# Kernel optimization log

Measured on AMD Instinct MI355X. Metric: run time of the kernel, lower is better.

Reference implementation:

```python
import jax, jax.numpy as jnp
import numpy as np

NUM_HEADS = 4
NUM_POINTS = 8


def deform_attn_3d(q, value, ref, Hf, Wf, Wv, bv, Wo, bo, Wa, ba):
    # q: (BS,N,C)  value: (BS,Hf*Wf,C)  ref: (BS,N,D,2) normalized (x,y) in [0,1]
    BS, N, C = q.shape
    H, P = NUM_HEADS, NUM_POINTS
    D = ref.shape[2]
    c = C // H
    # value projection, split heads: (BS,H,M,c)
    v = (value @ Wv + bv).reshape(BS, Hf * Wf, H, c).transpose(0, 2, 1, 3)
    # sampling offsets and attention weights from the query
    off = (q @ Wo + bo).reshape(BS, N, H, P, 2)
    attn = jax.nn.softmax((q @ Wa + ba).reshape(BS, N, H, P), axis=-1)
    # normalize offsets by (W,H); distribute P points over D z-anchors (P//D per anchor)
    norm = jnp.array([Wf, Hf], dtype=q.dtype)
    off = off.reshape(BS, N, H, P // D, D, 2) / norm
    loc = (ref[:, :, None, None, :, :] + off).reshape(BS, N, H, P, 2)
    # grid_sample(align_corners=False, padding=zeros): pixel = loc*size - 0.5
    x = loc[..., 0] * Wf - 0.5
    y = loc[..., 1] * Hf - 0.5
    x0f = jnp.floor(x)
    y0f = jnp.floor(y)
    lx = x - x0f
    ly = y - y0f
    x0 = x0f.astype(jnp.int32)
    y0 = y0f.astype(jnp.int32)

    def tohead(a):  # (BS,N,H,P) -> (BS,H,N*P)
        return a.transpose(0, 2, 1, 3).reshape(BS, H, N * P)

    def gather(yy, xx):
        valid = ((xx >= 0) & (xx < Wf) & (yy >= 0) & (yy < Hf)).astype(q.dtype)
        idx = jnp.clip(yy, 0, Hf - 1) * Wf + jnp.clip(xx, 0, Wf - 1)
        g = jnp.take_along_axis(v, tohead(idx)[..., None], axis=2)  # (BS,H,N*P,c)
        return g * tohead(valid)[..., None]

    out = (gather(y0, x0) * tohead((1 - lx) * (1 - ly))[..., None]
           + gather(y0, x0 + 1) * tohead(lx * (1 - ly))[..., None]
           + gather(y0 + 1, x0) * tohead((1 - lx) * ly)[..., None]
           + gather(y0 + 1, x0 + 1) * tohead(lx * ly)[..., None])
    out = (out * tohead(attn)[..., None]).reshape(BS, H, N, P, c).sum(3)  # (BS,H,N,c)
    return out.transpose(0, 2, 1, 3).reshape(BS, N, C)


def spatial_cross_attention(query, query_pos, value, reference_points_cam, bev_mask,
                            Hf, Wf, Wv, bv, Wo, bo, Wa, ba, Wout, bout):
    # query/query_pos: (B,N,C); value: (S,M,B,C); ref: (S,B,N,D,2); bev_mask: (S,B,N,D)
    B, N, C = query.shape
    S, M = value.shape[0], value.shape[1]
    D = reference_points_cam.shape[3]
    q = query + query_pos
    # broadcast queries over cameras (mask-equivalent of the torch rebatch/compaction):
    # deformable attention is per-query independent, so computing all queries per cam
    # and masking invalid ones is the same math as rebatch+scatter.
    q_all = jnp.broadcast_to(q[:, None], (B, S, N, C)).reshape(B * S, N, C)
    v_all = value.transpose(2, 0, 1, 3).reshape(B * S, M, C)
    ref = reference_points_cam.transpose(1, 0, 2, 3, 4).reshape(B * S, N, D, 2)
    out = deform_attn_3d(q_all, v_all, ref, Hf, Wf, Wv, bv, Wo, bo, Wa, ba)
    out = out.reshape(B, S, N, C)
    mask_q = (bev_mask.sum(-1) > 0).astype(query.dtype)  # (S,B,N): query hits this cam
    slots = (out * mask_q.transpose(1, 0, 2)[..., None]).sum(1)  # (B,N,C)
    count = jnp.maximum(mask_q.sum(0), 1.0)  # (B,N) clamp(min=1)
    slots = slots / count[..., None]
    # output_proj, dropout (eval -> identity), residual with original query
    return slots @ Wout + bout + query


def setup_inputs() -> dict:
    B, S, N, Z, C = 1, 6, 16384, 8, 128
    Hf, Wf = 28, 50
    H, P = NUM_HEADS, NUM_POINTS
    rng = jax.random.key(0)
    ks = jax.random.split(rng, 12)
    return {
        "query": jax.random.normal(ks[0], (B, N, C), jnp.float32),
        "query_pos": 0.1 * jax.random.normal(ks[1], (B, N, C), jnp.float32),
        "value": jax.random.normal(ks[2], (S, Hf * Wf, B, C), jnp.float32),
        "reference_points_cam": jax.random.uniform(ks[3], (S, B, N, Z, 2), jnp.float32),
        "bev_mask": jax.random.randint(ks[4], (S, B, N, Z), 0, 2).astype(bool),
        "Wv": 0.02 * jax.random.normal(ks[5], (C, C), jnp.float32),
        "bv": jnp.zeros((C,), jnp.float32),
        "Wo": 0.02 * jax.random.normal(ks[6], (C, H * P * 2), jnp.float32),
        "bo": 0.5 * jax.random.normal(ks[7], (H * P * 2,), jnp.float32),
        "Wa": 0.02 * jax.random.normal(ks[8], (C, H * P), jnp.float32),
        "ba": jnp.zeros((H * P,), jnp.float32),
        "Wout": 0.02 * jax.random.normal(ks[9], (C, C), jnp.float32),
        "bout": jnp.zeros((C,), jnp.float32),
        "Hf": Hf,
        "Wf": Wf,
    }


def reference(query, query_pos, value, reference_points_cam, bev_mask,
              Wv, bv, Wo, bo, Wa, ba, Wout, bout, Hf, Wf):
    return spatial_cross_attention(query, query_pos, value, reference_points_cam, bev_mask,
                                   Hf, Wf, Wv, bv, Wo, bo, Wa, ba, Wout, bout)
```

## Files before the change

kernel.cpp:

```cpp
#include <hip/hip_runtime.h>

#define N_Q   16384
#define C_DIM 128
#define S_CAM 6
#define M_VAL 1400
#define D_Z   8
#define HF    28
#define WF    50
#define QPB   16

typedef float f32x2 __attribute__((ext_vector_type(2)));

__device__ __forceinline__ bool mask_any(const unsigned char* __restrict__ mask,
                                         int mflag, size_t mbase){
  if(mflag==0){
    int any=0;
    #pragma unroll
    for(int d=0;d<D_Z;d++) any |= mask[mbase+d];
    return any!=0;
  } else if(mflag==1){
    const int* mp = (const int*)mask;  int any=0;
    #pragma unroll
    for(int d=0;d<D_Z;d++) any |= mp[mbase+d];
    return any!=0;
  } else {
    const long long* mp = (const long long*)mask;  long long any=0;
    #pragma unroll
    for(int d=0;d<D_Z;d++) any |= mp[mbase+d];
    return any!=0;
  }
}

__device__ __forceinline__ void corner_acc(const uint4 cv, const float wgt,
                                           float* __restrict__ acc){
  const unsigned dw[4] = {cv.x, cv.y, cv.z, cv.w};
  #pragma unroll
  for(int j=0;j<4;j++){
    const f32x2 lo = __builtin_amdgcn_cvt_pk_f32_fp8(dw[j], false);
    const f32x2 hi = __builtin_amdgcn_cvt_pk_f32_fp8(dw[j], true);
    acc[j*4+0] += wgt*lo[0];  acc[j*4+1] += wgt*lo[1];
    acc[j*4+2] += wgt*hi[0];  acc[j*4+3] += wgt*hi[1];
  }
}

__global__ __launch_bounds__(256)
void value_proj_kernel(const float* __restrict__ value,
                       const float* __restrict__ Wv,
                       const float* __restrict__ bv,
                       unsigned char* __restrict__ v8,
                       const unsigned char* __restrict__ mask,
                       int* __restrict__ flag){
  __shared__ float tile[8][C_DIM];
  __shared__ int s_cntA, s_cntB;
  const int tid = threadIdx.x;
  const int col = tid & 127;
  const int rh  = tid >> 7;
  const int r0  = blockIdx.x * 8;
  if(blockIdx.x==0 && tid==0){ s_cntA=0; s_cntB=0; }
  {
    const float4* src = (const float4*)(value + (size_t)r0*C_DIM);
    ((float4*)&tile[0][0])[tid] = src[tid];
  }
  __syncthreads();
  float acc[4];
  const float bias = bv[col];
  #pragma unroll
  for(int r=0;r<4;r++) acc[r]=bias;
  for(int k=0;k<C_DIM;k+=4){
    const float w0 = Wv[(k+0)*C_DIM + col];
    const float w1 = Wv[(k+1)*C_DIM + col];
    const float w2 = Wv[(k+2)*C_DIM + col];
    const float w3 = Wv[(k+3)*C_DIM + col];
    #pragma unroll
    for(int r=0;r<4;r++){
      const float4 t = *(const float4*)&tile[rh*4+r][k];
      acc[r] += t.x*w0 + t.y*w1 + t.z*w2 + t.w*w3;
    }
  }
  #pragma unroll
  for(int r=0;r<4;r++){
    const int pk = __builtin_amdgcn_cvt_pk_fp8_f32(acc[r], acc[r], 0, false);
    v8[(size_t)(r0+rh*4+r)*C_DIM + col] = (unsigned char)(pk & 0xff);
  }
  if(blockIdx.x==0){
    int a=0, b=0;
    for(int i=tid;i<1024;i+=256){
      const unsigned char v = mask[i];
      if(((i&3)!=0) && v) a=1;
      if(((i&7)==4) && v) b=1;
    }
    if(a) atomicOr(&s_cntA,1);
    if(b) atomicOr(&s_cntB,1);
    __syncthreads();
    if(tid==0) flag[0] = s_cntA ? 0 : (s_cntB ? 1 : 2);
  }
}

__global__ __launch_bounds__(256)
void fused_deform_kernel(const unsigned char* __restrict__ v8,
                         const float* __restrict__ query,
                         const float* __restrict__ query_pos,
                         const float* __restrict__ Wo, const float* __restrict__ bo,
                         const float* __restrict__ Wa, const float* __restrict__ ba,
                         const float* __restrict__ ref,
                         const unsigned char* __restrict__ mask,
                         const int* __restrict__ flag,
                         const float* __restrict__ Wout,
                         const float* __restrict__ bout,
                         float* __restrict__ out){
  __shared__ float  qs[QPB][C_DIM+4];
  __shared__ float  offs[QPB][68];
  __shared__ float  attns[QPB][36];
  __shared__ float  logits[QPB][36];
  __shared__ float2 refs[QPB][S_CAM*D_Z+1];
  __shared__ int    activ[QPB][S_CAM];
  __shared__ float  cinv[QPB];

  const int tid = threadIdx.x;
  const int n0  = blockIdx.x * QPB;
  const int mflag = flag[0];
  const int qi = tid >> 4;
  const int l  = tid & 15;

  float2 rpre[3];
  #pragma unroll
  for(int j=0;j<3;j++){
    const int e = tid + 256*j;
    const int q = e/48, r = e%48;
    rpre[j] = ((const float2*)ref)[((size_t)(r>>3)*N_Q + (n0+q))*D_Z + (r&7)];
  }

  {
    const float4* qa = (const float4*)(query     + (size_t)n0*C_DIM);
    const float4* qb = (const float4*)(query_pos + (size_t)n0*C_DIM);
    #pragma unroll
    for(int j=0;j<2;j++){
      const int idx = tid + 256*j;
      const int r = idx >> 5, c4 = idx & 31;
      float4 A = qa[idx], B = qb[idx];
      *(float4*)&qs[r][c4*4] = make_float4(A.x+B.x, A.y+B.y, A.z+B.z, A.w+B.w);
    }
  }
  __syncthreads();

  {
    float ao0 = bo[l*4+0], ao1 = bo[l*4+1], ao2 = bo[l*4+2], ao3 = bo[l*4+3];
    float aa0 = ba[l*2+0], aa1 = ba[l*2+1];
    for(int k=0;k<C_DIM;k++){
      const float qv = qs[qi][k];
      const float4 wo = *(const float4*)&Wo[k*64 + l*4];
      const float2 wa = *(const float2*)&Wa[k*32 + l*2];
      ao0 += qv*wo.x; ao1 += qv*wo.y; ao2 += qv*wo.z; ao3 += qv*wo.w;
      aa0 += qv*wa.x; aa1 += qv*wa.y;
    }
    offs[qi][l*4+0] = ao0;  offs[qi][l*4+1] = ao1;
    offs[qi][l*4+2] = ao2;  offs[qi][l*4+3] = ao3;
    logits[qi][l*2+0] = aa0;  logits[qi][l*2+1] = aa1;
  }
  #pragma unroll
  for(int j=0;j<3;j++){
    const int e = tid + 256*j;
    refs[e/48][e%48] = rpre[j];
  }
  if(tid < QPB*S_CAM){
    const int q2 = tid / S_CAM, s = tid % S_CAM;
    activ[q2][s] = mask_any(mask, mflag, ((size_t)s*N_Q + (n0+q2))*D_Z) ? 1 : 0;
  }
  __syncthreads();
  if(tid < 64){
    const int q2 = tid >> 2, h = tid & 3;
    const float* L = &logits[q2][h*8];
    float mx = L[0];
    #pragma unroll
    for(int p=1;p<8;p++) mx = fmaxf(mx, L[p]);
    float e[8], ssum = 0.f;
    #pragma unroll
    for(int p=0;p<8;p++){ e[p] = __expf(L[p]-mx); ssum += e[p]; }
    const float inv = 1.f/ssum;
    #pragma unroll
    for(int p=0;p<8;p++) attns[q2][h*8+p] = e[p]*inv;
  } else if(tid >= 256-QPB){
    const int q2 = tid - (256-QPB);
    int c = 0;
    #pragma unroll
    for(int s=0;s<S_CAM;s++) c += activ[q2][s];
    cinv[q2] = 1.f / fmaxf((float)c, 1.f);
  }
  __syncthreads();

  const int sg  = l >> 3;
  const int ll  = l & 7;
  const int gch = ll*16;
  const int gh  = ll >> 1;
  float acc[16];
  #pragma unroll
  for(int i=0;i<16;i++) acc[i]=0.f;

  for(int s=sg*3; s<sg*3+3; s++){
    if(!activ[qi][s]) continue;
    const unsigned char* vb = v8 + (size_t)s*M_VAL*C_DIM + gch;
    #pragma unroll 2
    for(int p=0;p<8;p++){
      const float2 r2 = refs[qi][s*8+p];
      const float ox = offs[qi][gh*16+p*2+0];
      const float oy = offs[qi][gh*16+p*2+1];
      const float x = fmaf(r2.x, (float)WF, ox - 0.5f);
      const float y = fmaf(r2.y, (float)HF, oy - 0.5f);
      const float x0f = floorf(x), y0f = floorf(y);
      const float fx = x - x0f,    fy = y - y0f;
      const int x0 = (int)x0f, y0 = (int)y0f;
      const int x1 = x0+1,     y1 = y0+1;
      const float at = attns[qi][gh*8+p];
      const float wx0 = (x0>=0 && x0<WF) ? (1.f-fx) : 0.f;
      const float wx1 = (x1>=0 && x1<WF) ? fx       : 0.f;
      const float wy0 = ((y0>=0 && y0<HF) ? (1.f-fy) : 0.f) * at;
      const float wy1 = ((y1>=0 && y1<HF) ? fy       : 0.f) * at;
      const int x0c = min(max(x0,0), WF-1), x1c = min(max(x1,0), WF-1);
      const int y0c = min(max(y0,0), HF-1), y1c = min(max(y1,0), HF-1);
      const float w00 = wx0*wy0, w01 = wx1*wy0, w10 = wx0*wy1, w11 = wx1*wy1;
      const uint4 c00 = *(const uint4*)(vb + (size_t)(y0c*WF+x0c)*C_DIM);
      const uint4 c01 = *(const uint4*)(vb + (size_t)(y0c*WF+x1c)*C_DIM);
      const uint4 c10 = *(const uint4*)(vb + (size_t)(y1c*WF+x0c)*C_DIM);
      const uint4 c11 = *(const uint4*)(vb + (size_t)(y1c*WF+x1c)*C_DIM);
      corner_acc(c00, w00, acc);
      corner_acc(c01, w01, acc);
      corner_acc(c10, w10, acc);
      corner_acc(c11, w11, acc);
    }
  }

  __syncthreads();
  if(sg==0){
    #pragma unroll
    for(int i=0;i<4;i++)
      *(float4*)&qs[qi][gch+i*4] = *(const float4*)&acc[i*4];
  }
  __syncthreads();
  if(sg==1){
    const float inv = cinv[qi];
    #pragma unroll
    for(int i=0;i<4;i++){
      float4 pA = *(const float4*)&qs[qi][gch+i*4];
      *(float4*)&qs[qi][gch+i*4] = make_float4((pA.x+acc[i*4+0])*inv,
                                               (pA.y+acc[i*4+1])*inv,
                                               (pA.z+acc[i*4+2])*inv,
                                               (pA.w+acc[i*4+3])*inv);
    }
  }
  __syncthreads();
  {
    const int c0 = l*8;
    const int n  = n0 + qi;
    const float4 bA = *(const float4*)&bout[c0];
    const float4 bB = *(const float4*)&bout[c0+4];
    const float4 rA = *(const float4*)&query[(size_t)n*C_DIM + c0];
    const float4 rB = *(const float4*)&query[(size_t)n*C_DIM + c0 + 4];
    float o0=bA.x+rA.x, o1=bA.y+rA.y, o2=bA.z+rA.z, o3=bA.w+rA.w;
    float o4=bB.x+rB.x, o5=bB.y+rB.y, o6=bB.z+rB.z, o7=bB.w+rB.w;
    for(int k=0;k<C_DIM;k++){
      const float sv = qs[qi][k];
      const float4 wA = *(const float4*)&Wout[(size_t)k*C_DIM + c0];
      const float4 wB = *(const float4*)&Wout[(size_t)k*C_DIM + c0 + 4];
      o0 += sv*wA.x; o1 += sv*wA.y; o2 += sv*wA.z; o3 += sv*wA.w;
      o4 += sv*wB.x; o5 += sv*wB.y; o6 += sv*wB.z; o7 += sv*wB.w;
    }
    *(float4*)&out[(size_t)n*C_DIM + c0]     = make_float4(o0,o1,o2,o3);
    *(float4*)&out[(size_t)n*C_DIM + c0 + 4] = make_float4(o4,o5,o6,o7);
  }
}

extern "C" void kernel_launch(void* const* d_in, const int* in_sizes, int n_in,
                              void* d_out, int out_size, void* d_ws, size_t ws_size,
                              hipStream_t stream){
  const float* query     = (const float*)d_in[0];
  const float* query_pos = (const float*)d_in[1];
  const float* value     = (const float*)d_in[2];
  const float* ref       = (const float*)d_in[3];
  const unsigned char* mask = (const unsigned char*)d_in[4];
  const float* Wv   = (const float*)d_in[5];
  const float* bv   = (const float*)d_in[6];
  const float* Wo   = (const float*)d_in[7];
  const float* bo   = (const float*)d_in[8];
  const float* Wa   = (const float*)d_in[9];
  const float* ba   = (const float*)d_in[10];
  const float* Wout = (const float*)d_in[11];
  const float* bout = (const float*)d_in[12];
  float* out = (float*)d_out;

  int* flag = (int*)d_ws;
  unsigned char* v8 = (unsigned char*)((char*)d_ws + 64);

  value_proj_kernel<<<(S_CAM*M_VAL)/8, 256, 0, stream>>>(value, Wv, bv, v8, mask, flag);
  fused_deform_kernel<<<N_Q/QPB, 256, 0, stream>>>(v8, query, query_pos,
                                                   Wo, bo, Wa, ba, ref, mask, flag,
                                                   Wout, bout, out);
}
```

Measured before the change: 186.5 us.

## Stage per-head camera feature maps in LDS and split output projection into separate kernel

Restructures the gather so each block handles 128 queries for a single head and stages each camera's fp8 value slice for that head in shared memory, turning random global corner loads into LDS reads. The sampled, count-normalized result is written as fp16 to a workspace buffer, and a new out_proj kernel applies Wout, the bias and the residual. The goal is to cut scattered global/L2 gather traffic, at the cost of one extra kernel launch, an fp16 round trip through memory, repeated per-camera LDS fills, and larger LDS use per block that lowers occupancy. Camera masking now zeroes the attention weights instead of skipping the camera, so every camera's work is executed.

```diff
diff --git a/kernel.cpp b/kernel.cpp
--- a/kernel.cpp
+++ b/kernel.cpp
@@ -1,4 +1,5 @@
 #include <hip/hip_runtime.h>
+#include <hip/hip_fp16.h>
 
 #define N_Q   16384
 #define C_DIM 128
@@ -7,7 +8,8 @@
 #define D_Z   8
 #define HF    28
 #define WF    50
-#define QPB   16
+#define QT    128
+#define CSTR  48
 
 typedef float f32x2 __attribute__((ext_vector_type(2)));
 
@@ -97,79 +99,66 @@
 }
 
 __global__ __launch_bounds__(256)
-void fused_deform_kernel(const unsigned char* __restrict__ v8,
-                         const float* __restrict__ query,
-                         const float* __restrict__ query_pos,
-                         const float* __restrict__ Wo, const float* __restrict__ bo,
-                         const float* __restrict__ Wa, const float* __restrict__ ba,
-                         const float* __restrict__ ref,
-                         const unsigned char* __restrict__ mask,
-                         const int* __restrict__ flag,
-                         const float* __restrict__ Wout,
-                         const float* __restrict__ bout,
-                         float* __restrict__ out){
-  __shared__ float  qs[QPB][C_DIM+4];
-  __shared__ float  offs[QPB][68];
-  __shared__ float  attns[QPB][36];
-  __shared__ float  logits[QPB][36];
-  __shared__ float2 refs[QPB][S_CAM*D_Z+1];
-  __shared__ int    activ[QPB][S_CAM];
-  __shared__ float  cinv[QPB];
+void gather_kernel(const unsigned char* __restrict__ v8,
+                   const float* __restrict__ query,
+                   const float* __restrict__ query_pos,
+                   const float* __restrict__ Wo, const float* __restrict__ bo,
+                   const float* __restrict__ Wa, const float* __restrict__ ba,
+                   const float* __restrict__ ref,
+                   const unsigned char* __restrict__ mask,
+                   const int* __restrict__ flag,
+                   unsigned short* __restrict__ slots16){
+  __shared__ union {
+    struct {
+      float qsL[32][132];
+      float logitsL[128][9];
+    } pre;
+    unsigned char cam[M_VAL*CSTR];
+  } U;
+  __shared__ float offsL[128][17];
+  __shared__ float attnL[128][8];
+  __shared__ float cinvL[128];
+  __shared__ unsigned char activL[128][8];
 
   const int tid = threadIdx.x;
-  const int n0  = blockIdx.x * QPB;
+  const int h   = blockIdx.x & 3;
+  const int n0  = (blockIdx.x >> 2) * QT;
   const int mflag = flag[0];
-  const int qi = tid >> 4;
-  const int l  = tid & 15;
-
-  float2 rpre[3];
-  #pragma unroll
-  for(int j=0;j<3;j++){
-    const int e = tid + 256*j;
-    const int q = e/48, r = e%48;
-    rpre[j] = ((const float2*)ref)[((size_t)(r>>3)*N_Q + (n0+q))*D_Z + (r&7)];
-  }
-
-  {
-    const float4* qa = (const float4*)(query     + (size_t)n0*C_DIM);
-    const float4* qb = (const float4*)(query_pos + (size_t)n0*C_DIM);
-    #pragma unroll
-    for(int j=0;j<2;j++){
-      const int idx = tid + 256*j;
-      const int r = idx >> 5, c4 = idx & 31;
-      float4 A = qa[idx], B = qb[idx];
-      *(float4*)&qs[r][c4*4] = make_float4(A.x+B.x, A.y+B.y, A.z+B.z, A.w+B.w);
-    }
-  }
-  __syncthreads();
-
-  {
-    float ao0 = bo[l*4+0], ao1 = bo[l*4+1], ao2 = bo[l*4+2], ao3 = bo[l*4+3];
-    float aa0 = ba[l*2+0], aa1 = ba[l*2+1];
-    for(int k=0;k<C_DIM;k++){
-      const float qv = qs[qi][k];
-      const float4 wo = *(const float4*)&Wo[k*64 + l*4];
-      const float2 wa = *(const float2*)&Wa[k*32 + l*2];
-      ao0 += qv*wo.x; ao1 += qv*wo.y; ao2 += qv*wo.z; ao3 += qv*wo.w;
-      aa0 += qv*wa.x; aa1 += qv*wa.y;
-    }
-    offs[qi][l*4+0] = ao0;  offs[qi][l*4+1] = ao1;
-    offs[qi][l*4+2] = ao2;  offs[qi][l*4+3] = ao3;
-    logits[qi][l*2+0] = aa0;  logits[qi][l*2+1] = aa1;
-  }
-  #pragma unroll
-  for(int j=0;j<3;j++){
-    const int e = tid + 256*j;
-    refs[e/48][e%48] = rpre[j];
-  }
-  if(tid < QPB*S_CAM){
-    const int q2 = tid / S_CAM, s = tid % S_CAM;
-    activ[q2][s] = mask_any(mask, mflag, ((size_t)s*N_Q + (n0+q2))*D_Z) ? 1 : 0;
-  }
-  __syncthreads();
-  if(tid < 64){
-    const int q2 = tid >> 2, h = tid & 3;
-    const float* L = &logits[q2][h*8];
+
+  const int pq = tid >> 3;
+  const int pj = tid & 7;
+  for(int c=0;c<4;c++){
+    {
+      const float4* qa = (const float4*)(query     + (size_t)(n0 + c*32)*C_DIM);
+      const float4* qb = (const float4*)(query_pos + (size_t)(n0 + c*32)*C_DIM);
+      #pragma unroll
+      for(int i=0;i<4;i++){
+        const int idx = tid + 256*i;
+        const int r = idx >> 5, cc = idx & 31;
+        float4 A = qa[idx], B = qb[idx];
+        *(float4*)&U.pre.qsL[r][cc*4] = make_float4(A.x+B.x, A.y+B.y, A.z+B.z, A.w+B.w);
+      }
+    }
+    __syncthreads();
+    {
+      float ao0 = bo[h*16 + pj*2], ao1 = bo[h*16 + pj*2 + 1];
+      float aa  = ba[h*8 + pj];
+      for(int k=0;k<C_DIM;k++){
+        const float qv = U.pre.qsL[pq][k];
+        const float2 wo = *(const float2*)&Wo[k*64 + h*16 + pj*2];
+        ao0 += qv*wo.x; ao1 += qv*wo.y;
+        aa  += qv*Wa[k*32 + h*8 + pj];
+      }
+      const int q = c*32 + pq;
+      offsL[q][pj*2]   = ao0;
+      offsL[q][pj*2+1] = ao1;
+      U.pre.logitsL[q][pj] = aa;
+    }
+    __syncthreads();
+  }
+  if(tid < 128){
+    const int q = tid;
+    const float* L = U.pre.logitsL[q];
     float mx = L[0];
     #pragma unroll
     for(int p=1;p<8;p++) mx = fmaxf(mx, L[p]);
@@ -178,94 +167,126 @@
     for(int p=0;p<8;p++){ e[p] = __expf(L[p]-mx); ssum += e[p]; }
     const float inv = 1.f/ssum;
     #pragma unroll
-    for(int p=0;p<8;p++) attns[q2][h*8+p] = e[p]*inv;
-  } else if(tid >= 256-QPB){
-    const int q2 = tid - (256-QPB);
-    int c = 0;
-    #pragma unroll
-    for(int s=0;s<S_CAM;s++) c += activ[q2][s];
-    cinv[q2] = 1.f / fmaxf((float)c, 1.f);
+    for(int p=0;p<8;p++) attnL[q][p] = e[p]*inv;
+    int cnt = 0;
+    #pragma unroll
+    for(int s=0;s<S_CAM;s++){
+      const bool a = mask_any(mask, mflag, ((size_t)s*N_Q + (n0+q))*D_Z);
+      activL[q][s] = a ? 1 : 0;
+      cnt += a ? 1 : 0;
+    }
+    cinvL[q] = 1.f / fmaxf((float)cnt, 1.f);
   }
   __syncthreads();
 
-  const int sg  = l >> 3;
-  const int ll  = l & 7;
-  const int gch = ll*16;
-  const int gh  = ll >> 1;
+  const int gq = tid >> 1, cg = tid & 1;
+  const int n  = n0 + gq;
   float acc[16];
   #pragma unroll
   for(int i=0;i<16;i++) acc[i]=0.f;
 
-  for(int s=sg*3; s<sg*3+3; s++){
-    if(!activ[qi][s]) continue;
-    const unsigned char* vb = v8 + (size_t)s*M_VAL*C_DIM + gch;
-    #pragma unroll 2
-    for(int p=0;p<8;p++){
-      const float2 r2 = refs[qi][s*8+p];
-      const float ox = offs[qi][gh*16+p*2+0];
-      const float oy = offs[qi][gh*16+p*2+1];
-      const float x = fmaf(r2.x, (float)WF, ox - 0.5f);
-      const float y = fmaf(r2.y, (float)HF, oy - 0.5f);
-      const float x0f = floorf(x), y0f = floorf(y);
-      const float fx = x - x0f,    fy = y - y0f;
-      const int x0 = (int)x0f, y0 = (int)y0f;
-      const int x1 = x0+1,     y1 = y0+1;
-      const float at = attns[qi][gh*8+p];
-      const float wx0 = (x0>=0 && x0<WF) ? (1.f-fx) : 0.f;
-      const float wx1 = (x1>=0 && x1<WF) ? fx       : 0.f;
-      const float wy0 = ((y0>=0 && y0<HF) ? (1.f-fy) : 0.f) * at;
-      const float wy1 = ((y1>=0 && y1<HF) ? fy       : 0.f) * at;
-      const int x0c = min(max(x0,0), WF-1), x1c = min(max(x1,0), WF-1);
-      const int y0c = min(max(y0,0), HF-1), y1c = min(max(y1,0), HF-1);
-      const float w00 = wx0*wy0, w01 = wx1*wy0, w10 = wx0*wy1, w11 = wx1*wy1;
-      const uint4 c00 = *(const uint4*)(vb + (size_t)(y0c*WF+x0c)*C_DIM);
-      const uint4 c01 = *(const uint4*)(vb + (size_t)(y0c*WF+x1c)*C_DIM);
-      const uint4 c10 = *(const uint4*)(vb + (size_t)(y1c*WF+x0c)*C_DIM);
-      const uint4 c11 = *(const uint4*)(vb + (size_t)(y1c*WF+x1c)*C_DIM);
-      corner_acc(c00, w00, acc);
-      corner_acc(c01, w01, acc);
-      corner_acc(c10, w10, acc);
-      corner_acc(c11, w11, acc);
-    }
-  }
-
+  for(int s=0;s<S_CAM;s++){
+    #pragma unroll
+    for(int i=0;i<6;i++){
+      const int r = i*256 + tid;
+      if(r < M_VAL){
+        const unsigned char* src = v8 + ((size_t)s*M_VAL + r)*C_DIM + h*32;
+        const uint4 w0 = *(const uint4*)(src);
+        const uint4 w1 = *(const uint4*)(src + 16);
+        *(uint4*)&U.cam[r*CSTR]      = w0;
+        *(uint4*)&U.cam[r*CSTR + 16] = w1;
+      }
+    }
+    __syncthreads();
+    {
+      const float actf = activL[gq][s] ? 1.f : 0.f;
+      const float2* refp = (const float2*)ref + ((size_t)s*N_Q + n)*D_Z;
+      #pragma unroll 2
+      for(int p=0;p<8;p++){
+        const float2 r2 = refp[p];
+        const float ox = offsL[gq][p*2+0];
+        const float oy = offsL[gq][p*2+1];
+        const float x = fmaf(r2.x, (float)WF, ox - 0.5f);
+        const float y = fmaf(r2.y, (float)HF, oy - 0.5f);
+        const float x0f = floorf(x), y0f = floorf(y);
+        const float fx = x - x0f,    fy = y - y0f;
+        const int x0 = (int)x0f, y0 = (int)y0f;
+        const int x1 = x0+1,     y1 = y0+1;
+        const float at = attnL[gq][p] * actf;
+        const float wx0 = (x0>=0 && x0<WF) ? (1.f-fx) : 0.f;
+        const float wx1 = (x1>=0 && x1<WF) ? fx       : 0.f;
+        const float wy0 = ((y0>=0 && y0<HF) ? (1.f-fy) : 0.f) * at;
+        const float wy1 = ((y1>=0 && y1<HF) ? fy       : 0.f) * at;
+        const int x0c = min(max(x0,0), WF-1), x1c = min(max(x1,0), WF-1);
+        const int y0c = min(max(y0,0), HF-1), y1c = min(max(y1,0), HF-1);
+        const float w00 = wx0*wy0, w01 = wx1*wy0, w10 = wx0*wy1, w11 = wx1*wy1;
+        const int co = cg*16;
+        const uint4 c00 = *(const uint4*)&U.cam[(y0c*WF+x0c)*CSTR + co];
+        const uint4 c01 = *(const uint4*)&U.cam[(y0c*WF+x1c)*CSTR + co];
+        const uint4 c10 = *(const uint4*)&U.cam[(y1c*WF+x0c)*CSTR + co];
+        const uint4 c11 = *(const uint4*)&U.cam[(y1c*WF+x1c)*CSTR + co];
+        corner_acc(c00, w00, acc);
+        corner_acc(c01, w01, acc);
+        corner_acc(c10, w10, acc);
+        corner_acc(c11, w11, acc);
+      }
+    }
+    __syncthreads();
+  }
+
+  {
+    const float inv = cinvL[gq];
+    unsigned wds[8];
+    #pragma unroll
+    for(int j=0;j<8;j++){
+      const unsigned lo = __half_as_ushort(__float2half_rn(acc[2*j+0]*inv));
+      const unsigned hi = __half_as_ushort(__float2half_rn(acc[2*j+1]*inv));
+      wds[j] = lo | (hi << 16);
+    }
+    unsigned short* dst = slots16 + (size_t)n*C_DIM + h*32 + cg*16;
+    *(uint4*)(dst)     = make_uint4(wds[0], wds[1], wds[2], wds[3]);
+    *(uint4*)(dst + 8) = make_uint4(wds[4], wds[5], wds[6], wds[7]);
+  }
+}
+
+__global__ __launch_bounds__(256)
+void out_proj_kernel(const unsigned short* __restrict__ slots16,
+                     const float* __restrict__ Wout,
+                     const float* __restrict__ bout,
+                     const float* __restrict__ query,
+                     float* __restrict__ out){
+  __shared__ float tile[16][C_DIM];
+  const int tid = threadIdx.x;
+  const int r0  = blockIdx.x * 16;
+  {
+    const int row = tid >> 4, seg = tid & 15;
+    const uint4 u = *(const uint4*)(slots16 + (size_t)(r0+row)*C_DIM + seg*8);
+    const __half* hp = (const __half*)&u;
+    #pragma unroll
+    for(int j=0;j<8;j++) tile[row][seg*8+j] = __half2float(hp[j]);
+  }
   __syncthreads();
-  if(sg==0){
-    #pragma unroll
-    for(int i=0;i<4;i++)
-      *(float4*)&qs[qi][gch+i*4] = *(const float4*)&acc[i*4];
-  }
-  __syncthreads();
-  if(sg==1){
-    const float inv = cinv[qi];
-    #pragma unroll
-    for(int i=0;i<4;i++){
-      float4 pA = *(const float4*)&qs[qi][gch+i*4];
-      *(float4*)&qs[qi][gch+i*4] = make_float4((pA.x+acc[i*4+0])*inv,
-                                               (pA.y+acc[i*4+1])*inv,
-                                               (pA.z+acc[i*4+2])*inv,
-                                               (pA.w+acc[i*4+3])*inv);
-    }
-  }
-  __syncthreads();
-  {
-    const int c0 = l*8;
-    const int n  = n0 + qi;
-    const float4 bA = *(const float4*)&bout[c0];
-    const float4 bB = *(const float4*)&bout[c0+4];
-    const float4 rA = *(const float4*)&query[(size_t)n*C_DIM + c0];
-    const float4 rB = *(const float4*)&query[(size_t)n*C_DIM + c0 + 4];
-    float o0=bA.x+rA.x, o1=bA.y+rA.y, o2=bA.z+rA.z, o3=bA.w+rA.w;
-    float o4=bB.x+rB.x, o5=bB.y+rB.y, o6=bB.z+rB.z, o7=bB.w+rB.w;
-    for(int k=0;k<C_DIM;k++){
-      const float sv = qs[qi][k];
-      const float4 wA = *(const float4*)&Wout[(size_t)k*C_DIM + c0];
-      const float4 wB = *(const float4*)&Wout[(size_t)k*C_DIM + c0 + 4];
-      o0 += sv*wA.x; o1 += sv*wA.y; o2 += sv*wA.z; o3 += sv*wA.w;
-      o4 += sv*wB.x; o5 += sv*wB.y; o6 += sv*wB.z; o7 += sv*wB.w;
-    }
-    *(float4*)&out[(size_t)n*C_DIM + c0]     = make_float4(o0,o1,o2,o3);
-    *(float4*)&out[(size_t)n*C_DIM + c0 + 4] = make_float4(o4,o5,o6,o7);
+  const int col = tid & 127;
+  const int rh  = tid >> 7;
+  float acc[8];
+  const float bias = bout[col];
+  #pragma unroll
+  for(int r=0;r<8;r++) acc[r]=bias;
+  for(int k=0;k<C_DIM;k+=4){
+    const float w0 = Wout[(k+0)*C_DIM + col];
+    const float w1 = Wout[(k+1)*C_DIM + col];
+    const float w2 = Wout[(k+2)*C_DIM + col];
+    const float w3 = Wout[(k+3)*C_DIM + col];
+    #pragma unroll
+    for(int r=0;r<8;r++){
+      const float4 t = *(const float4*)&tile[rh*8+r][k];
+      acc[r] += t.x*w0 + t.y*w1 + t.z*w2 + t.w*w3;
+    }
+  }
+  #pragma unroll
+  for(int r=0;r<8;r++){
+    const size_t idx = (size_t)(r0+rh*8+r)*C_DIM + col;
+    out[idx] = acc[r] + query[idx];
   }
 }
 
@@ -288,10 +309,11 @@
   float* out = (float*)d_out;
 
   int* flag = (int*)d_ws;
-  unsigned char* v8 = (unsigned char*)((char*)d_ws + 64);
+  unsigned char*  v8      = (unsigned char*)((char*)d_ws + 64);
+  unsigned short* slots16 = (unsigned short*)((char*)d_ws + 64 + (size_t)S_CAM*M_VAL*C_DIM);
 
   value_proj_kernel<<<(S_CAM*M_VAL)/8, 256, 0, stream>>>(value, Wv, bv, v8, mask, flag);
-  fused_deform_kernel<<<N_Q/QPB, 256, 0, stream>>>(v8, query, query_pos,
-                                                   Wo, bo, Wa, ba, ref, mask, flag,
-                                                   Wout, bout, out);
-}
+  gather_kernel<<<(N_Q/QT)*4, 256, 0, stream>>>(v8, query, query_pos,
+                                                Wo, bo, Wa, ba, ref, mask, flag, slots16);
+  out_proj_kernel<<<N_Q/16, 256, 0, stream>>>(slots16, Wout, bout, query, out);
+}
```

New measurement: 221.7 us. +18.8%, slower.
